# Optimization experiments

Hardware: AMD Instinct MI355X
Metric: run time of the kernel (lower is better)

Reference implementation:

```python
import jax, jax.numpy as jnp
import numpy as np

N, L, D_IN = 8192, 32, 256   # total paths, max path len, token+method embed
E, H, T, C = 128, 128, 128, 2  # encode_size, hidden_dim, test_vector_size, label_count
G = 1024                      # number of methods (groups)
LN_EPS = 1e-5


def _lstm_last_hidden(xs, lengths, Wih, Whh, bih, bhh):
    """Single-layer LSTM over padded [N,L,E]; returns h at t=length-1 per row (packed-sequence h_n)."""
    xs_t = jnp.transpose(xs, (1, 0, 2))  # [L, N, E]
    n = xs.shape[0]
    h0 = jnp.zeros((n, H), xs.dtype)
    c0 = jnp.zeros((n, H), xs.dtype)

    def step(carry, inp):
        h, c = carry
        x_t, t = inp
        gates = x_t @ Wih.T + bih + h @ Whh.T + bhh  # [N, 4H], torch gate order i,f,g,o
        i, f, g, o = jnp.split(gates, 4, axis=-1)
        c_new = jax.nn.sigmoid(f) * c + jax.nn.sigmoid(i) * jnp.tanh(g)
        h_new = jax.nn.sigmoid(o) * jnp.tanh(c_new)
        valid = (t < lengths)[:, None]  # freeze state past each path's length
        return (jnp.where(valid, h_new, h), jnp.where(valid, c_new, c)), None

    (h_last, _), _ = jax.lax.scan(step, (h0, c0), (xs_t, jnp.arange(L)))
    return h_last  # [N, H]


def setup_inputs() -> dict:
    key = jax.random.key(0)
    ks = jax.random.split(key, 10)
    rng = np.random.default_rng(0)

    inputs = jax.random.normal(ks[0], (N, L, D_IN), dtype=jnp.float32)
    path_lengths = jnp.asarray(rng.integers(1, L + 1, size=N), dtype=jnp.int32)
    # sorted segment ids, every group non-empty (torch.split groups are contiguous and >=1)
    ids = np.sort(np.concatenate([np.arange(G), rng.integers(0, G, size=N - G)]))
    segment_ids = jnp.asarray(ids, dtype=jnp.int32)

    s = 0.05
    W_in = jax.random.normal(ks[1], (E, D_IN), dtype=jnp.float32) * s
    ln_gamma = jnp.ones((E,), jnp.float32)
    ln_beta = jnp.zeros((E,), jnp.float32)
    Wih = jax.random.normal(ks[2], (4 * H, E), dtype=jnp.float32) * s
    Whh = jax.random.normal(ks[3], (4 * H, H), dtype=jnp.float32) * s
    bih = jax.random.normal(ks[4], (4 * H,), dtype=jnp.float32) * s
    bhh = jax.random.normal(ks[5], (4 * H,), dtype=jnp.float32) * s
    attn_param = jax.random.normal(ks[6], (H,), dtype=jnp.float32) * s
    W_out = jax.random.normal(ks[7], (T, H), dtype=jnp.float32) * s
    W_cls = jax.random.normal(ks[8], (C, T), dtype=jnp.float32) * s

    return {"inputs": inputs, "path_lengths": path_lengths, "segment_ids": segment_ids,
            "W_in": W_in, "ln_gamma": ln_gamma, "ln_beta": ln_beta,
            "Wih": Wih, "Whh": Whh, "bih": bih, "bhh": bhh,
            "attn_param": attn_param, "W_out": W_out, "W_cls": W_cls}


def reference(inputs, path_lengths, segment_ids, W_in, ln_gamma, ln_beta,
              Wih, Whh, bih, bhh, attn_param, W_out, W_cls):
    # input projection + layernorm + tanh (dropout disabled, p=0)
    x = inputs @ W_in.T  # [N, L, E]
    mu = jnp.mean(x, axis=-1, keepdims=True)
    var = jnp.mean((x - mu) ** 2, axis=-1, keepdims=True)
    x = jnp.tanh((x - mu) * jax.lax.rsqrt(var + LN_EPS) * ln_gamma + ln_beta)

    h = _lstm_last_hidden(x, path_lengths, Wih, Whh, bih, bhh)  # [N, H]

    # segmented softmax attention + mean over each group's paths
    logits = h @ attn_param  # [N]
    m = jax.ops.segment_max(logits, segment_ids, num_segments=G)
    e = jnp.exp(logits - m[segment_ids])
    Z = jax.ops.segment_sum(e, segment_ids, num_segments=G)
    attn = e / Z[segment_ids]  # per-group softmax weights
    wsum = jax.ops.segment_sum(attn[:, None] * h, segment_ids, num_segments=G)  # [G, H]
    counts = jax.ops.segment_sum(jnp.ones_like(logits), segment_ids, num_segments=G)
    code = wsum / counts[:, None]  # torch.mean divides by group size

    code_vectors = code @ W_out.T  # [G, T]
    outputs = code_vectors @ W_cls.T  # [G, C]
    return outputs, code_vectors, attn_param
```

## Files before the change

kernel.cpp:

```cpp
#include <hip/hip_runtime.h>


#define NPATH 8192
#define LMAX  32
#define DIN   256
#define EDIM  128
#define HDIM  128
#define G4    512
#define NGRP  1024
#define NTOK  (NPATH * LMAX)

typedef __attribute__((ext_vector_type(8))) short short8;
typedef __attribute__((ext_vector_type(4))) short s16x4;
typedef __attribute__((ext_vector_type(4))) float f32x4;

__device__ __forceinline__ unsigned short f2bf(float f) {
    unsigned int x = __float_as_uint(f);
    x += 0x7fffu + ((x >> 16) & 1u);
    return (unsigned short)(x >> 16);
}
__device__ __forceinline__ float sigmoid_f(float x) {
    return __fdividef(1.f, 1.f + __expf(-x));
}
__device__ __forceinline__ float tanh_f(float x) {
    float ax = fabsf(x);
    float t = __expf(-2.f * ax);
    float r = __fdividef(1.f - t, 1.f + t);
    return copysignf(r, x);
}

#define K1_ROWS 128
#define K1_PAD  264
__global__ __launch_bounds__(512) void k1_proj(
    const float* __restrict__ inp, const float* __restrict__ Win,
    const float* __restrict__ gam, const float* __restrict__ bet,
    unsigned short* __restrict__ xt)
{
    __shared__ short As[K1_ROWS * K1_PAD];
    __shared__ short Bs[EDIM * K1_PAD];
    const int tid = threadIdx.x;
    const long m0 = (long)blockIdx.x * K1_ROWS;

    #pragma unroll
    for (int i = 0; i < 16; ++i) {
        int chunk = i * 512 + tid;
        int row = chunk >> 6, c4 = chunk & 63;
        float4 v = *(const float4*)&Win[row * DIN + c4 * 4];
        s16x4 s = { (short)f2bf(v.x), (short)f2bf(v.y), (short)f2bf(v.z), (short)f2bf(v.w) };
        *(s16x4*)&Bs[row * K1_PAD + c4 * 4] = s;
    }
    #pragma unroll
    for (int i = 0; i < 16; ++i) {
        int chunk = i * 512 + tid;
        int row = chunk >> 6, c4 = chunk & 63;
        float4 v = *(const float4*)&inp[(m0 + row) * DIN + c4 * 4];
        s16x4 s = { (short)f2bf(v.x), (short)f2bf(v.y), (short)f2bf(v.z), (short)f2bf(v.w) };
        *(s16x4*)&As[row * K1_PAD + c4 * 4] = s;
    }
    __syncthreads();

    const int w = tid >> 6, lane = tid & 63, q = lane >> 4, c = lane & 15;
    const f32x4 fzero = {0.f, 0.f, 0.f, 0.f};
    f32x4 acc[8];
    #pragma unroll
    for (int nt = 0; nt < 8; ++nt) acc[nt] = fzero;

    const short* arow = &As[(w * 16 + c) * K1_PAD + q * 8];
    const short* brow = &Bs[c * K1_PAD + q * 8];
    #pragma unroll
    for (int ks = 0; ks < 8; ++ks) {
        short8 a = *(const short8*)(arow + ks * 32);
        #pragma unroll
        for (int nt = 0; nt < 8; ++nt) {
            short8 b = *(const short8*)(brow + nt * 16 * K1_PAD + ks * 32);
            acc[nt] = __builtin_amdgcn_mfma_f32_16x16x32_bf16(a, b, acc[nt], 0, 0, 0);
        }
    }

    float gr[8], br[8];
    #pragma unroll
    for (int nt = 0; nt < 8; ++nt) { int col = nt * 16 + c; gr[nt] = gam[col]; br[nt] = bet[col]; }
    #pragma unroll
    for (int r = 0; r < 4; ++r) {
        float s = 0.f, ss = 0.f;
        #pragma unroll
        for (int nt = 0; nt < 8; ++nt) { float v = acc[nt][r]; s += v; ss += v * v; }
        #pragma unroll
        for (int m = 1; m < 16; m <<= 1) { s += __shfl_xor(s, m, 64); ss += __shfl_xor(ss, m, 64); }
        float mu = s * (1.f / 128.f);
        float var = ss * (1.f / 128.f) - mu * mu;
        float rstd = rsqrtf(var + 1e-5f);
        unsigned short* orow = &xt[(m0 + w * 16 + q * 4 + r) * EDIM];
        #pragma unroll
        for (int nt = 0; nt < 8; ++nt) {
            float v = (acc[nt][r] - mu) * rstd * gr[nt] + br[nt];
            orow[nt * 16 + c] = f2bf(tanh_f(v));
        }
    }
}

#define K2_PAD 136
__global__ __launch_bounds__(512) void k2_lstm(
    const unsigned short* __restrict__ xt,
    const float* __restrict__ Wih, const float* __restrict__ Whh,
    const float* __restrict__ bih, const float* __restrict__ bhh,
    const int* __restrict__ lens, float* __restrict__ h_last)
{
    __shared__ short Wh[G4 * K2_PAD];
    __shared__ short xb[32 * K2_PAD];
    __shared__ short hb[32 * K2_PAD];
    __shared__ int   lenb[32];
    const int tid = threadIdx.x;
    const int r0 = blockIdx.x * 32;

    #pragma unroll
    for (int i = 0; i < 32; ++i) {
        int chunk = i * 512 + tid;
        int row = chunk >> 5, c4 = chunk & 31;
        float4 v = *(const float4*)&Whh[row * HDIM + c4 * 4];
        s16x4 s = { (short)f2bf(v.x), (short)f2bf(v.y), (short)f2bf(v.z), (short)f2bf(v.w) };
        *(s16x4*)&Wh[row * K2_PAD + c4 * 4] = s;
    }
    for (int idx = tid; idx < 32 * K2_PAD; idx += 512) hb[idx] = 0;
    if (tid < 32) lenb[tid] = lens[r0 + tid];
    __syncthreads();

    const int w = tid >> 6, lane = tid & 63, q = lane >> 4, c = lane & 15;
    float bs[4];
    #pragma unroll
    for (int g_ = 0; g_ < 4; ++g_) { int j = g_ * 128 + w * 16 + c; bs[g_] = bih[j] + bhh[j]; }
    int lenr[2][4];
    #pragma unroll
    for (int mt = 0; mt < 2; ++mt)
        #pragma unroll
        for (int r = 0; r < 4; ++r) lenr[mt][r] = lenb[mt * 16 + q * 4 + r];

    short8 wf[4][4];
    #pragma unroll
    for (int g_ = 0; g_ < 4; ++g_) {
        const float* p = Wih + (g_ * 128 + w * 16 + c) * EDIM + q * 8;
        #pragma unroll
        for (int ks = 0; ks < 4; ++ks) {
            float4 u0 = *(const float4*)(p + ks * 32);
            float4 u1 = *(const float4*)(p + ks * 32 + 4);
            short8 s;
            s[0] = (short)f2bf(u0.x); s[1] = (short)f2bf(u0.y);
            s[2] = (short)f2bf(u0.z); s[3] = (short)f2bf(u0.w);
            s[4] = (short)f2bf(u1.x); s[5] = (short)f2bf(u1.y);
            s[6] = (short)f2bf(u1.z); s[7] = (short)f2bf(u1.w);
            wf[g_][ks] = s;
        }
    }
    const short* whb[4];
    #pragma unroll
    for (int g_ = 0; g_ < 4; ++g_) whb[g_] = &Wh[(g_ * 128 + w * 16 + c) * K2_PAD + q * 8];
    const short* xbb[2]; const short* hbb[2];
    #pragma unroll
    for (int mt = 0; mt < 2; ++mt) {
        xbb[mt] = &xb[(mt * 16 + c) * K2_PAD + q * 8];
        hbb[mt] = &hb[(mt * 16 + c) * K2_PAD + q * 8];
    }

    float c_reg[2][4] = {{0.f,0.f,0.f,0.f},{0.f,0.f,0.f,0.f}};
    float h_reg[2][4] = {{0.f,0.f,0.f,0.f},{0.f,0.f,0.f,0.f}};
    const f32x4 fzero = {0.f, 0.f, 0.f, 0.f};

    for (int t = 0; t < LMAX; ++t) {
        {
            int row = tid >> 4, c8 = tid & 15;
            *(short8*)&xb[row * K2_PAD + c8 * 8] =
                *(const short8*)&xt[((long)(r0 + row) * LMAX + t) * EDIM + c8 * 8];
        }
        __syncthreads();

        f32x4 acc[2][4];
        #pragma unroll
        for (int mt = 0; mt < 2; ++mt)
            #pragma unroll
            for (int g_ = 0; g_ < 4; ++g_) acc[mt][g_] = fzero;

        #pragma unroll
        for (int ks = 0; ks < 4; ++ks) {
            short8 a0 = *(const short8*)(hbb[0] + ks * 32);
            short8 a1 = *(const short8*)(hbb[1] + ks * 32);
            #pragma unroll
            for (int g_ = 0; g_ < 4; ++g_) {
                short8 b = *(const short8*)(whb[g_] + ks * 32);
                acc[0][g_] = __builtin_amdgcn_mfma_f32_16x16x32_bf16(a0, b, acc[0][g_], 0, 0, 0);
                acc[1][g_] = __builtin_amdgcn_mfma_f32_16x16x32_bf16(a1, b, acc[1][g_], 0, 0, 0);
            }
        }
        #pragma unroll
        for (int ks = 0; ks < 4; ++ks) {
            short8 a0 = *(const short8*)(xbb[0] + ks * 32);
            short8 a1 = *(const short8*)(xbb[1] + ks * 32);
            #pragma unroll
            for (int g_ = 0; g_ < 4; ++g_) {
                acc[0][g_] = __builtin_amdgcn_mfma_f32_16x16x32_bf16(a0, wf[g_][ks], acc[0][g_], 0, 0, 0);
                acc[1][g_] = __builtin_amdgcn_mfma_f32_16x16x32_bf16(a1, wf[g_][ks], acc[1][g_], 0, 0, 0);
            }
        }

        #pragma unroll
        for (int mt = 0; mt < 2; ++mt)
            #pragma unroll
            for (int r = 0; r < 4; ++r) {
                float iv = acc[mt][0][r] + bs[0];
                float fv = acc[mt][1][r] + bs[1];
                float gv = acc[mt][2][r] + bs[2];
                float ov = acc[mt][3][r] + bs[3];
                float cn = sigmoid_f(fv) * c_reg[mt][r] + sigmoid_f(iv) * tanh_f(gv);
                float hn = sigmoid_f(ov) * tanh_f(cn);
                if (t < lenr[mt][r]) { c_reg[mt][r] = cn; h_reg[mt][r] = hn; }
            }
        __syncthreads();
        #pragma unroll
        for (int mt = 0; mt < 2; ++mt)
            #pragma unroll
            for (int r = 0; r < 4; ++r)
                hb[(mt * 16 + q * 4 + r) * K2_PAD + w * 16 + c] = (short)f2bf(h_reg[mt][r]);
    }

    #pragma unroll
    for (int mt = 0; mt < 2; ++mt)
        #pragma unroll
        for (int r = 0; r < 4; ++r)
            h_last[(long)(r0 + mt * 16 + q * 4 + r) * HDIM + w * 16 + c] = h_reg[mt][r];
}

__global__ __launch_bounds__(64) void k3_attn(
    const float* __restrict__ h_last, const int* __restrict__ seg,
    const float* __restrict__ attn, const float* __restrict__ Wout,
    const float* __restrict__ Wcls, float* __restrict__ out)
{
    __shared__ float code_s[128];
    const int g = blockIdx.x, l = threadIdx.x;

    int lo, hi;
    { int a = 0, b = NPATH; while (a < b) { int m = (a + b) >> 1; if (seg[m] < g) a = m + 1; else b = m; } lo = a; }
    { int a = lo, b = NPATH; while (a < b) { int m = (a + b) >> 1; if (seg[m] < g + 1) a = m + 1; else b = m; } hi = a; }

    float a0 = attn[l], a1 = attn[l + 64];
    float mrun = -1e30f, Z = 0.f;
    for (int n = lo; n < hi; ++n) {
        const float* hr = &h_last[(long)n * HDIM];
        float v = hr[l] * a0 + hr[l + 64] * a1;
        #pragma unroll
        for (int m = 1; m < 64; m <<= 1) v += __shfl_xor(v, m, 64);
        float nm = fmaxf(mrun, v);
        Z = Z * __expf(mrun - nm) + __expf(v - nm);
        mrun = nm;
    }
    float w0 = 0.f, w1 = 0.f;
    for (int n = lo; n < hi; ++n) {
        const float* hr = &h_last[(long)n * HDIM];
        float v = hr[l] * a0 + hr[l + 64] * a1;
        #pragma unroll
        for (int m = 1; m < 64; m <<= 1) v += __shfl_xor(v, m, 64);
        float at = __expf(v - mrun) / Z;
        w0 += at * hr[l]; w1 += at * hr[l + 64];
    }
    float inv_cnt = (hi > lo) ? 1.f / (float)(hi - lo) : 0.f;
    code_s[l] = w0 * inv_cnt; code_s[l + 64] = w1 * inv_cnt;
    __syncthreads();

    float cv0 = 0.f, cv1 = 0.f;
    for (int k = 0; k < 128; ++k) {
        float ck = code_s[k];
        cv0 += ck * Wout[l * 128 + k];
        cv1 += ck * Wout[(l + 64) * 128 + k];
    }
    out[2048 + g * 128 + l]      = cv0;
    out[2048 + g * 128 + l + 64] = cv1;

    float p0 = cv0 * Wcls[l] + cv1 * Wcls[l + 64];
    float p1 = cv0 * Wcls[128 + l] + cv1 * Wcls[128 + l + 64];
    #pragma unroll
    for (int m = 1; m < 64; m <<= 1) { p0 += __shfl_xor(p0, m, 64); p1 += __shfl_xor(p1, m, 64); }
    if (l == 0) { out[g * 2 + 0] = p0; out[g * 2 + 1] = p1; }
    if (g == 0) { out[133120 + l] = attn[l]; out[133120 + 64 + l] = attn[l + 64]; }
}

extern "C" void kernel_launch(void* const* d_in, const int* in_sizes, int n_in,
                              void* d_out, int out_size, void* d_ws, size_t ws_size,
                              hipStream_t stream) {
    const float* inp  = (const float*)d_in[0];
    const int*   lens = (const int*)d_in[1];
    const int*   seg  = (const int*)d_in[2];
    const float* Win  = (const float*)d_in[3];
    const float* gam  = (const float*)d_in[4];
    const float* bet  = (const float*)d_in[5];
    const float* Wih  = (const float*)d_in[6];
    const float* Whh  = (const float*)d_in[7];
    const float* bih  = (const float*)d_in[8];
    const float* bhh  = (const float*)d_in[9];
    const float* attn = (const float*)d_in[10];
    const float* Wout = (const float*)d_in[11];
    const float* Wcls = (const float*)d_in[12];

    unsigned short* xt = (unsigned short*)d_ws;
    float* h_last = (float*)((char*)d_ws + (size_t)NTOK * EDIM * 2);

    hipLaunchKernelGGL(k1_proj, dim3(NTOK / K1_ROWS), dim3(512), 0, stream, inp, Win, gam, bet, xt);
    hipLaunchKernelGGL(k2_lstm, dim3(NPATH / 32), dim3(512), 0, stream, xt, Wih, Whh, bih, bhh, lens, h_last);
    hipLaunchKernelGGL(k3_attn, dim3(NGRP), dim3(64), 0, stream, h_last, seg, attn, Wout, Wcls,
                       (float*)d_out);
}
```

Measured before the change: 583.6 us.

## Sort paths by length and truncate LSTM steps per chunk with register weights

Adds a single-block counting sort that orders paths by length. The LSTM kernel now processes 16-row chunks in length order, running only up to the chunk's maximum length instead of all 32 steps. Each block handles a short chunk and a long chunk paired from opposite ends to balance load. Whh moves from LDS into registers, x tiles are prefetched straight from global memory, and h goes through a swizzled double-buffered LDS with one barrier per step. The cost is an extra launch, a serial single-block sort, and higher register pressure under launch_bounds(512,2).

```diff
diff --git a/kernel.cpp b/kernel.cpp
--- a/kernel.cpp
+++ b/kernel.cpp
@@ -6,9 +6,9 @@
 #define DIN   256
 #define EDIM  128
 #define HDIM  128
-#define G4    512
 #define NGRP  1024
 #define NTOK  (NPATH * LMAX)
+#define NCHUNK 512
 
 typedef __attribute__((ext_vector_type(8))) short short8;
 typedef __attribute__((ext_vector_type(4))) short s16x4;
@@ -27,6 +27,26 @@
     float t = __expf(-2.f * ax);
     float r = __fdividef(1.f - t, 1.f + t);
     return copysignf(r, x);
+}
+
+__global__ __launch_bounds__(512) void k0_sort(const int* __restrict__ lens,
+                                               int* __restrict__ perm) {
+    __shared__ int hist[LMAX];
+    __shared__ int offs[LMAX];
+    const int tid = threadIdx.x;
+    if (tid < LMAX) hist[tid] = 0;
+    __syncthreads();
+    for (int i = tid; i < NPATH; i += 512) atomicAdd(&hist[lens[i] - 1], 1);
+    __syncthreads();
+    if (tid == 0) {
+        int s = 0;
+        for (int b = 0; b < LMAX; ++b) { offs[b] = s; s += hist[b]; }
+    }
+    __syncthreads();
+    for (int i = tid; i < NPATH; i += 512) {
+        int p = atomicAdd(&offs[lens[i] - 1], 1);
+        perm[p] = i;
+    }
 }
 
 #define K1_ROWS 128
@@ -99,133 +119,119 @@
     }
 }
 
-#define K2_PAD 136
-__global__ __launch_bounds__(512) void k2_lstm(
+__global__ __launch_bounds__(512, 2) void k2_lstm(
     const unsigned short* __restrict__ xt,
     const float* __restrict__ Wih, const float* __restrict__ Whh,
     const float* __restrict__ bih, const float* __restrict__ bhh,
-    const int* __restrict__ lens, float* __restrict__ h_last)
+    const int* __restrict__ lens, const int* __restrict__ perm,
+    float* __restrict__ h_last)
 {
-    __shared__ short Wh[G4 * K2_PAD];
-    __shared__ short xb[32 * K2_PAD];
-    __shared__ short hb[32 * K2_PAD];
-    __shared__ int   lenb[32];
+    __shared__ unsigned short hb[2][16 * 128];
+    __shared__ int pemb[16];
+    __shared__ int lenb[16];
     const int tid = threadIdx.x;
-    const int r0 = blockIdx.x * 32;
-
-    #pragma unroll
-    for (int i = 0; i < 32; ++i) {
-        int chunk = i * 512 + tid;
-        int row = chunk >> 5, c4 = chunk & 31;
-        float4 v = *(const float4*)&Whh[row * HDIM + c4 * 4];
-        s16x4 s = { (short)f2bf(v.x), (short)f2bf(v.y), (short)f2bf(v.z), (short)f2bf(v.w) };
-        *(s16x4*)&Wh[row * K2_PAD + c4 * 4] = s;
-    }
-    for (int idx = tid; idx < 32 * K2_PAD; idx += 512) hb[idx] = 0;
-    if (tid < 32) lenb[tid] = lens[r0 + tid];
-    __syncthreads();
-
     const int w = tid >> 6, lane = tid & 63, q = lane >> 4, c = lane & 15;
+    const int xr = (c & 7) << 3;
+
+    short8 wf[4][4], whf[4][4];
     float bs[4];
     #pragma unroll
-    for (int g_ = 0; g_ < 4; ++g_) { int j = g_ * 128 + w * 16 + c; bs[g_] = bih[j] + bhh[j]; }
-    int lenr[2][4];
-    #pragma unroll
-    for (int mt = 0; mt < 2; ++mt)
-        #pragma unroll
-        for (int r = 0; r < 4; ++r) lenr[mt][r] = lenb[mt * 16 + q * 4 + r];
-
-    short8 wf[4][4];
-    #pragma unroll
-    for (int g_ = 0; g_ < 4; ++g_) {
-        const float* p = Wih + (g_ * 128 + w * 16 + c) * EDIM + q * 8;
+    for (int g = 0; g < 4; ++g) {
+        const int j = g * 128 + w * 16 + c;
+        bs[g] = bih[j] + bhh[j];
+        const float* pi = Wih + (long)j * EDIM + q * 8;
+        const float* ph = Whh + (long)j * HDIM + q * 8;
         #pragma unroll
         for (int ks = 0; ks < 4; ++ks) {
-            float4 u0 = *(const float4*)(p + ks * 32);
-            float4 u1 = *(const float4*)(p + ks * 32 + 4);
+            float4 a0 = *(const float4*)(pi + ks * 32);
+            float4 a1 = *(const float4*)(pi + ks * 32 + 4);
             short8 s;
-            s[0] = (short)f2bf(u0.x); s[1] = (short)f2bf(u0.y);
-            s[2] = (short)f2bf(u0.z); s[3] = (short)f2bf(u0.w);
-            s[4] = (short)f2bf(u1.x); s[5] = (short)f2bf(u1.y);
-            s[6] = (short)f2bf(u1.z); s[7] = (short)f2bf(u1.w);
-            wf[g_][ks] = s;
+            s[0] = (short)f2bf(a0.x); s[1] = (short)f2bf(a0.y);
+            s[2] = (short)f2bf(a0.z); s[3] = (short)f2bf(a0.w);
+            s[4] = (short)f2bf(a1.x); s[5] = (short)f2bf(a1.y);
+            s[6] = (short)f2bf(a1.z); s[7] = (short)f2bf(a1.w);
+            wf[g][ks] = s;
+            float4 b0 = *(const float4*)(ph + ks * 32);
+            float4 b1 = *(const float4*)(ph + ks * 32 + 4);
+            short8 u;
+            u[0] = (short)f2bf(b0.x); u[1] = (short)f2bf(b0.y);
+            u[2] = (short)f2bf(b0.z); u[3] = (short)f2bf(b0.w);
+            u[4] = (short)f2bf(b1.x); u[5] = (short)f2bf(b1.y);
+            u[6] = (short)f2bf(b1.z); u[7] = (short)f2bf(b1.w);
+            whf[g][ks] = u;
         }
     }
-    const short* whb[4];
-    #pragma unroll
-    for (int g_ = 0; g_ < 4; ++g_) whb[g_] = &Wh[(g_ * 128 + w * 16 + c) * K2_PAD + q * 8];
-    const short* xbb[2]; const short* hbb[2];
-    #pragma unroll
-    for (int mt = 0; mt < 2; ++mt) {
-        xbb[mt] = &xb[(mt * 16 + c) * K2_PAD + q * 8];
-        hbb[mt] = &hb[(mt * 16 + c) * K2_PAD + q * 8];
-    }
-
-    float c_reg[2][4] = {{0.f,0.f,0.f,0.f},{0.f,0.f,0.f,0.f}};
-    float h_reg[2][4] = {{0.f,0.f,0.f,0.f},{0.f,0.f,0.f,0.f}};
-    const f32x4 fzero = {0.f, 0.f, 0.f, 0.f};
-
-    for (int t = 0; t < LMAX; ++t) {
-        {
-            int row = tid >> 4, c8 = tid & 15;
-            *(short8*)&xb[row * K2_PAD + c8 * 8] =
-                *(const short8*)&xt[((long)(r0 + row) * LMAX + t) * EDIM + c8 * 8];
-        }
+
+    #pragma unroll
+    for (int half = 0; half < 2; ++half) {
+        const int cid = half ? (NCHUNK - 1 - (int)blockIdx.x) : (int)blockIdx.x;
+        const int r0 = cid * 16;
+        if (tid < 16) { int p = perm[r0 + tid]; pemb[tid] = p; lenb[tid] = lens[p]; }
+        { s16x4 z = {0, 0, 0, 0}; *(s16x4*)&hb[0][tid * 4] = z; }
         __syncthreads();
 
-        f32x4 acc[2][4];
-        #pragma unroll
-        for (int mt = 0; mt < 2; ++mt)
+        int steps = 1;
+        #pragma unroll
+        for (int i = 0; i < 16; ++i) steps = (lenb[i] > steps) ? lenb[i] : steps;
+        int lenr[4];
+        #pragma unroll
+        for (int r = 0; r < 4; ++r) lenr[r] = lenb[q * 4 + r];
+        const unsigned short* xrow = xt + (long)pemb[c] * (LMAX * EDIM) + q * 8;
+
+        float c_reg[4] = {0.f, 0.f, 0.f, 0.f};
+        float h_reg[4] = {0.f, 0.f, 0.f, 0.f};
+        short8 xf[4];
+        #pragma unroll
+        for (int ks = 0; ks < 4; ++ks) xf[ks] = *(const short8*)(xrow + ks * 32);
+
+        int cur = 0;
+        for (int t = 0; t < steps; ++t) {
+            f32x4 acc[4];
             #pragma unroll
-            for (int g_ = 0; g_ < 4; ++g_) acc[mt][g_] = fzero;
-
-        #pragma unroll
-        for (int ks = 0; ks < 4; ++ks) {
-            short8 a0 = *(const short8*)(hbb[0] + ks * 32);
-            short8 a1 = *(const short8*)(hbb[1] + ks * 32);
+            for (int g = 0; g < 4; ++g) {
+                f32x4 a = {bs[g], bs[g], bs[g], bs[g]};
+                acc[g] = a;
+            }
+            if (t) {
+                short8 ha[4];
+                #pragma unroll
+                for (int ks = 0; ks < 4; ++ks)
+                    ha[ks] = *(const short8*)&hb[cur][c * 128 + ((q * 8 + ks * 32) ^ xr)];
+                #pragma unroll
+                for (int ks = 0; ks < 4; ++ks)
+                    #pragma unroll
+                    for (int g = 0; g < 4; ++g)
+                        acc[g] = __builtin_amdgcn_mfma_f32_16x16x32_bf16(ha[ks], whf[g][ks], acc[g], 0, 0, 0);
+            }
             #pragma unroll
-            for (int g_ = 0; g_ < 4; ++g_) {
-                short8 b = *(const short8*)(whb[g_] + ks * 32);
-                acc[0][g_] = __builtin_amdgcn_mfma_f32_16x16x32_bf16(a0, b, acc[0][g_], 0, 0, 0);
-                acc[1][g_] = __builtin_amdgcn_mfma_f32_16x16x32_bf16(a1, b, acc[1][g_], 0, 0, 0);
+            for (int ks = 0; ks < 4; ++ks)
+                #pragma unroll
+                for (int g = 0; g < 4; ++g)
+                    acc[g] = __builtin_amdgcn_mfma_f32_16x16x32_bf16(xf[ks], wf[g][ks], acc[g], 0, 0, 0);
+            {
+                const int tn = (t + 1 < steps) ? (t + 1) : t;
+                const unsigned short* xp = xrow + (long)tn * EDIM;
+                #pragma unroll
+                for (int ks = 0; ks < 4; ++ks) xf[ks] = *(const short8*)(xp + ks * 32);
             }
-        }
-        #pragma unroll
-        for (int ks = 0; ks < 4; ++ks) {
-            short8 a0 = *(const short8*)(xbb[0] + ks * 32);
-            short8 a1 = *(const short8*)(xbb[1] + ks * 32);
-            #pragma unroll
-            for (int g_ = 0; g_ < 4; ++g_) {
-                acc[0][g_] = __builtin_amdgcn_mfma_f32_16x16x32_bf16(a0, wf[g_][ks], acc[0][g_], 0, 0, 0);
-                acc[1][g_] = __builtin_amdgcn_mfma_f32_16x16x32_bf16(a1, wf[g_][ks], acc[1][g_], 0, 0, 0);
-            }
-        }
-
-        #pragma unroll
-        for (int mt = 0; mt < 2; ++mt)
+            const int nxt = cur ^ 1;
             #pragma unroll
             for (int r = 0; r < 4; ++r) {
-                float iv = acc[mt][0][r] + bs[0];
-                float fv = acc[mt][1][r] + bs[1];
-                float gv = acc[mt][2][r] + bs[2];
-                float ov = acc[mt][3][r] + bs[3];
-                float cn = sigmoid_f(fv) * c_reg[mt][r] + sigmoid_f(iv) * tanh_f(gv);
-                float hn = sigmoid_f(ov) * tanh_f(cn);
-                if (t < lenr[mt][r]) { c_reg[mt][r] = cn; h_reg[mt][r] = hn; }
+                float cn = sigmoid_f(acc[1][r]) * c_reg[r]
+                         + sigmoid_f(acc[0][r]) * tanh_f(acc[2][r]);
+                float hn = sigmoid_f(acc[3][r]) * tanh_f(cn);
+                if (t < lenr[r]) { c_reg[r] = cn; h_reg[r] = hn; }
+                const int row = q * 4 + r;
+                hb[nxt][row * 128 + ((w * 16 + c) ^ ((row & 7) << 3))] = f2bf(h_reg[r]);
             }
-        __syncthreads();
-        #pragma unroll
-        for (int mt = 0; mt < 2; ++mt)
-            #pragma unroll
-            for (int r = 0; r < 4; ++r)
-                hb[(mt * 16 + q * 4 + r) * K2_PAD + w * 16 + c] = (short)f2bf(h_reg[mt][r]);
-    }
-
-    #pragma unroll
-    for (int mt = 0; mt < 2; ++mt)
+            __syncthreads();
+            cur = nxt;
+        }
         #pragma unroll
         for (int r = 0; r < 4; ++r)
-            h_last[(long)(r0 + mt * 16 + q * 4 + r) * HDIM + w * 16 + c] = h_reg[mt][r];
+            h_last[(long)pemb[q * 4 + r] * HDIM + w * 16 + c] = h_reg[r];
+        if (half == 0) __syncthreads();
+    }
 }
 
 __global__ __launch_bounds__(64) void k3_attn(
@@ -300,9 +306,13 @@
 
     unsigned short* xt = (unsigned short*)d_ws;
     float* h_last = (float*)((char*)d_ws + (size_t)NTOK * EDIM * 2);
-
+    int* perm = (int*)((char*)d_ws + (size_t)NTOK * EDIM * 2
+                                   + (size_t)NPATH * HDIM * 4);
+
+    hipLaunchKernelGGL(k0_sort, dim3(1), dim3(512), 0, stream, lens, perm);
     hipLaunchKernelGGL(k1_proj, dim3(NTOK / K1_ROWS), dim3(512), 0, stream, inp, Win, gam, bet, xt);
-    hipLaunchKernelGGL(k2_lstm, dim3(NPATH / 32), dim3(512), 0, stream, xt, Wih, Whh, bih, bhh, lens, h_last);
+    hipLaunchKernelGGL(k2_lstm, dim3(NCHUNK / 2), dim3(512), 0, stream,
+                       xt, Wih, Whh, bih, bhh, lens, perm, h_last);
     hipLaunchKernelGGL(k3_attn, dim3(NGRP), dim3(64), 0, stream, h_last, seg, attn, Wout, Wcls,
                        (float*)d_out);
 }
```

Result: faster. 545.7 us (-6.5%).
